# Kernel tuning notes

Measured on AMD Instinct MI355X. Metric: run time of the kernel, lower is better.

## Reference

```python
import jax, jax.numpy as jnp
import numpy as np

B, H, W, C = 64, 14, 14, 768

def setup_inputs() -> dict:
    key = jax.random.key(0)
    k = jax.random.split(key, 5)
    s = 0.02  # small init so tanh/sigmoid stay in active range
    return {
        "x": jax.random.normal(k[0], (B, H, W, C), dtype=jnp.float32),
        "Wx": jax.random.normal(k[1], (3 * C, C), dtype=jnp.float32) * s,
        "bx": jnp.zeros((3 * C,), dtype=jnp.float32),
        "Wh": jax.random.normal(k[2], (3 * C, C), dtype=jnp.float32) * s,
        "bh": jnp.zeros((3 * C,), dtype=jnp.float32),
        "Wp": jax.random.normal(k[3], (C, C), dtype=jnp.float32) * s,
    }

def reference(x, Wx, bx, Wh, bh, Wp):
    b, h_, w_, c = x.shape
    n = h_ * w_
    seq = x.reshape(b, n, c)
    # Input projections for all timesteps at once (no recurrent dependency).
    x_zrn = jnp.einsum('bnc,dc->bnd', seq, Wx) + bx  # [B, N, 3C]
    x_zrn_t = jnp.transpose(x_zrn, (1, 0, 2))        # [N, B, 3C] for scan

    def step(h, xz):
        h_zrn = h @ Wh.T + bh                         # [B, 3C]
        x_z, x_r, x_n = jnp.split(xz, 3, axis=-1)
        h_z, h_r, h_n = jnp.split(h_zrn, 3, axis=-1)
        z = jax.nn.sigmoid(x_z + h_z)
        r = jax.nn.sigmoid(x_r + h_r)
        ncand = jnp.tanh(x_n + r * h_n)
        h_new = (1.0 - z) * ncand + z * h
        return h_new, h_new

    h0 = jnp.zeros((b, c), dtype=x.dtype)
    _, hs = jax.lax.scan(step, h0, x_zrn_t)           # hs: [N, B, C]
    y = jnp.transpose(hs, (1, 0, 2))                  # [B, N, C]
    y = jnp.einsum('bnc,dc->bnd', y, Wp)              # proj (no bias)
    # proj_drop = 0.0 -> identity
    return y.reshape(b, h_, w_, c)
```

## Files before the change

kernel.cpp:

```cpp
#include <hip/hip_runtime.h>

typedef unsigned short u16;
typedef unsigned int   u32;
typedef unsigned long long u64;
typedef __attribute__((ext_vector_type(8))) short bf16x8;
typedef __attribute__((ext_vector_type(4))) float f32x4;

#define GK 768
#define NSTEP 196
#define HSTEP 49152
#define PWG 24
#define NGRP 8
#define NBLK 256
#define FLINE 32
#define FLAG0 64
#define MIR0 6656
#define GUARD (1 << 18)

__device__ __forceinline__ u16 f2bf(float f) {
    u32 u = __float_as_uint(f);
    u = (u + 0x7fffu + ((u >> 16) & 1u)) >> 16;
    return (u16)u;
}
__device__ __forceinline__ float bf2f(u16 h) { return __uint_as_float(((u32)h) << 16); }

__device__ __forceinline__ int agent_load(const int* p) {
    return __hip_atomic_load(p, __ATOMIC_RELAXED, __HIP_MEMORY_SCOPE_AGENT);
}
__device__ __forceinline__ void agent_store(int* p, int v) {
    __hip_atomic_store(p, v, __ATOMIC_RELAXED, __HIP_MEMORY_SCOPE_AGENT);
}
__device__ __forceinline__ int atomic_read_l2(int* p) {
    int v; int zero = 0;
    asm volatile("global_atomic_add %0, %1, %2, off sc0\n\t"
                 "s_waitcnt vmcnt(0)"
                 : "=&v"(v) : "v"(p), "v"(zero) : "memory");
    return v;
}

__global__ __launch_bounds__(256) void cvt_kernel(
    const float4* __restrict__ x, const float4* __restrict__ wx,
    const float4* __restrict__ wp,
    u32* __restrict__ xb, u32* __restrict__ wxb, u32* __restrict__ wpb,
    int* __restrict__ flags)
{
    const int N1 = 9633792 / 4, N2 = 1769472 / 4;
    int i = blockIdx.x * 256 + threadIdx.x;
    if (blockIdx.x < 32) flags[blockIdx.x * 256 + threadIdx.x] = 0;
    const float4* src; u32* dst; int off;
    if (i < N1)            { src = x;  dst = xb;  off = i; }
    else if (i < N1 + N2)  { src = wx; dst = wxb; off = i - N1; }
    else                   { src = wp; dst = wpb; off = i - N1 - N2; }
    float4 v = src[off];
    u32 lo = (u32)f2bf(v.x) | ((u32)f2bf(v.y) << 16);
    u32 hi = (u32)f2bf(v.z) | ((u32)f2bf(v.w) << 16);
    dst[(size_t)off * 2]     = lo;
    dst[(size_t)off * 2 + 1] = hi;
}

template<int MODE>
__global__ __launch_bounds__(256) void gemm_bt(
    const u16* __restrict__ A, const u16* __restrict__ B,
    const float* __restrict__ bias, void* __restrict__ outv)
{
    __shared__ u16 As[128 * 40];
    __shared__ u16 Bs[128 * 40];
    const int tid  = threadIdx.x;
    const int lane = tid & 63;
    const int wv   = tid >> 6;
    const int m0 = blockIdx.y * 128;
    const int n0 = blockIdx.x * 128;
    const int wm = (wv & 1) * 64;
    const int wn = (wv >> 1) * 64;

    f32x4 acc[4][4];
#pragma unroll
    for (int i = 0; i < 4; ++i)
#pragma unroll
        for (int j = 0; j < 4; ++j) acc[i][j] = (f32x4){0.f, 0.f, 0.f, 0.f};

    const int r0 = tid >> 2, q0 = tid & 3;
    const u16* gA0 = A + (size_t)(m0 + r0)      * GK + q0 * 8;
    const u16* gA1 = A + (size_t)(m0 + r0 + 64) * GK + q0 * 8;
    const u16* gB0 = B + (size_t)(n0 + r0)      * GK + q0 * 8;
    const u16* gB1 = B + (size_t)(n0 + r0 + 64) * GK + q0 * 8;
    u16* sA0 = As + r0 * 40 + q0 * 8;
    u16* sA1 = As + (r0 + 64) * 40 + q0 * 8;
    u16* sB0 = Bs + r0 * 40 + q0 * 8;
    u16* sB1 = Bs + (r0 + 64) * 40 + q0 * 8;

    const int fr = lane & 15, fq = lane >> 4;
    const u16* fA = As + (wm + fr) * 40 + fq * 8;
    const u16* fB = Bs + (wn + fr) * 40 + fq * 8;

    for (int kt = 0; kt < GK / 32; ++kt) {
        uint4 a0 = *(const uint4*)(gA0 + kt * 32);
        uint4 a1 = *(const uint4*)(gA1 + kt * 32);
        uint4 b0 = *(const uint4*)(gB0 + kt * 32);
        uint4 b1 = *(const uint4*)(gB1 + kt * 32);
        __syncthreads();
        *(uint4*)sA0 = a0; *(uint4*)sA1 = a1;
        *(uint4*)sB0 = b0; *(uint4*)sB1 = b1;
        __syncthreads();
        bf16x8 af[4], bfr[4];
#pragma unroll
        for (int mi = 0; mi < 4; ++mi) af[mi]  = *(const bf16x8*)(fA + mi * 16 * 40);
#pragma unroll
        for (int ni = 0; ni < 4; ++ni) bfr[ni] = *(const bf16x8*)(fB + ni * 16 * 40);
#pragma unroll
        for (int mi = 0; mi < 4; ++mi)
#pragma unroll
            for (int ni = 0; ni < 4; ++ni)
                acc[mi][ni] = __builtin_amdgcn_mfma_f32_16x16x32_bf16(
                    af[mi], bfr[ni], acc[mi][ni], 0, 0, 0);
    }

    if (MODE == 1) {
        u16* out = (u16*)outv;
#pragma unroll
        for (int mi = 0; mi < 4; ++mi) {
#pragma unroll
            for (int ni = 0; ni < 4; ++ni) {
                int col = n0 + wn + ni * 16 + fr;
                float bv = bias[col];
#pragma unroll
                for (int r = 0; r < 4; ++r) {
                    int m = m0 + wm + mi * 16 + fq * 4 + r;
                    int b = m / 196;
                    int nn = m - b * 196;
                    u16 hv = f2bf(acc[mi][ni][r] + bv);
                    int other = __shfl_xor((int)hv, 1, 64);
                    if (!(lane & 1)) {
                        u32 packed = (u32)hv | (((u32)(u16)other) << 16);
                        size_t eidx = ((size_t)nn * 64 + (size_t)b) * 2304 + (size_t)col;
                        *((u32*)out + (eidx >> 1)) = packed;
                    }
                }
            }
        }
    } else {
        float* out = (float*)outv;
#pragma unroll
        for (int mi = 0; mi < 4; ++mi) {
#pragma unroll
            for (int ni = 0; ni < 4; ++ni) {
                int col = n0 + wn + ni * 16 + fr;
#pragma unroll
                for (int r = 0; r < 4; ++r) {
                    int m = m0 + wm + mi * 16 + fq * 4 + r;
                    int b = m & 63;
                    int nn = m >> 6;
                    out[((size_t)b * 196 + nn) * 768 + col] = acc[mi][ni][r];
                }
            }
        }
    }
}

template<bool FAST>
__device__ void recur_core(
    int g, int s, int tid,
    const u16* __restrict__ xz, const float* __restrict__ Wh,
    const float* __restrict__ bh, u16* __restrict__ hsx, int* flags,
    float* hzs)
{
    const int lane = tid & 63;
    const int wv   = tid >> 6;
    const int kh   = wv & 1;
    const int np   = wv >> 1;
    const int fr   = lane & 15, fq = lane >> 4;
    const int c0   = s * 32;
    const int B0   = g * 8;

    bf16x8 bfrag[2][12];
#pragma unroll
    for (int j = 0; j < 2; ++j) {
        int row = np * 768 + c0 + j * 16 + fr;
        const float* wp = Wh + (size_t)row * 768 + kh * 384 + fq * 8;
#pragma unroll
        for (int kk = 0; kk < 12; ++kk) {
            float4 f0 = *(const float4*)(wp + kk * 32);
            float4 f1 = *(const float4*)(wp + kk * 32 + 4);
            bf16x8 b;
            b[0] = (short)f2bf(f0.x); b[1] = (short)f2bf(f0.y);
            b[2] = (short)f2bf(f0.z); b[3] = (short)f2bf(f0.w);
            b[4] = (short)f2bf(f1.x); b[5] = (short)f2bf(f1.y);
            b[6] = (short)f2bf(f1.z); b[7] = (short)f2bf(f1.w);
            bfrag[j][kk] = b;
        }
    }

    const int gb = tid >> 5, gi = tid & 31;
    const int gc = c0 + gi;
    float bh0 = 0.f, bh1 = 0.f, bh2 = 0.f, hold = 0.f;
    if (tid < 256) { bh0 = bh[gc]; bh1 = bh[768 + gc]; bh2 = bh[1536 + gc]; }

    const int pl = lane % PWG;
    int* const myflag = &flags[FLAG0 + (g * PWG + s)  * FLINE];
    int* const pollp  = &flags[FLAG0 + (g * PWG + pl) * FLINE];
    int* const mymir  = &flags[MIR0 + g * FLINE + s];
    const int* const pollm = &flags[MIR0 + g * FLINE + pl];

    float xgn0 = 0.f, xgn1 = 0.f, xgn2 = 0.f;
    if (tid < 256) {
        size_t xoff = (size_t)(B0 + gb) * 2304 + gc;
        xgn0 = bf2f(xz[xoff]);
        xgn1 = bf2f(xz[xoff + 768]);
        xgn2 = bf2f(xz[xoff + 1536]);
    }

    bool slow = !FAST;

    for (int n = 0; n < NSTEP; ++n) {
        const float xg0 = xgn0, xg1 = xgn1, xg2 = xgn2;

        f32x4 acc0 = (f32x4){0.f, 0.f, 0.f, 0.f};
        f32x4 acc1 = (f32x4){0.f, 0.f, 0.f, 0.f};

        if (n > 0) {
            if (tid >= 320) {
                bool done = false;
                if (FAST && !slow) {
                    int tries = 0;
                    for (;;) {
                        int v = atomic_read_l2(pollp);
                        if (__all(v >= n)) { done = true; break; }
                        if (++tries > 4096) { slow = true; break; }
                        __builtin_amdgcn_s_sleep(1);
                    }
                }
                if (!done) {
                    int guard = 0;
                    for (;;) {
                        int v = agent_load(pollm);
                        if (__all(v >= n)) break;
                        if (++guard > GUARD) break;
                        __builtin_amdgcn_s_sleep(1);
                    }
                }
            }
            __syncthreads();

            const u16* ap = hsx + (size_t)(n - 1) * HSTEP
                                + (size_t)(B0 + fr) * 768 + kh * 384 + fq * 8;
            const bool arow = fr < 8;
#pragma unroll
            for (int kk = 0; kk < 12; ++kk) {
                bf16x8 a = arow ? *(const bf16x8*)(ap + kk * 32)
                                : (bf16x8){0, 0, 0, 0, 0, 0, 0, 0};
                acc0 = __builtin_amdgcn_mfma_f32_16x16x32_bf16(a, bfrag[0][kk], acc0, 0, 0, 0);
                acc1 = __builtin_amdgcn_mfma_f32_16x16x32_bf16(a, bfrag[1][kk], acc1, 0, 0, 0);
            }
        }

#pragma unroll
        for (int r = 0; r < 4; ++r) {
            int b = fq * 4 + r;
            if (b < 8) {
                hzs[(kh * 8 + b) * 96 + np * 32 + fr]      = acc0[r];
                hzs[(kh * 8 + b) * 96 + np * 32 + 16 + fr] = acc1[r];
            }
        }
        __syncthreads();

        if (tid < 256) {
            float h0 = hzs[gb * 96 + gi]      + hzs[(8 + gb) * 96 + gi]      + bh0;
            float h1 = hzs[gb * 96 + 32 + gi] + hzs[(8 + gb) * 96 + 32 + gi] + bh1;
            float h2 = hzs[gb * 96 + 64 + gi] + hzs[(8 + gb) * 96 + 64 + gi] + bh2;
            float z   = 1.f / (1.f + __expf(-(xg0 + h0)));
            float rr2 = 1.f / (1.f + __expf(-(xg1 + h1)));
            float pre = xg2 + rr2 * h2;
            float e2  = __expf(-2.f * pre);
            float nc  = (1.f - e2) / (1.f + e2);
            float hnew = (1.f - z) * nc + z * hold;
            hold = hnew;

            u16 hv = f2bf(hnew);
            u32 other = ((u32)__shfl_xor((int)hv, 1, 64)) & 0xffffu;
            u32 v01 = (u32)hv | (other << 16);
            u32 v23 = (u32)__shfl_xor((int)v01, 2, 64);
            if ((tid & 3) == 0) {
                u64 q = (u64)v01 | ((u64)v23 << 32);
                size_t ofs = (size_t)n * HSTEP + (size_t)(B0 + gb) * 768 + gc;
                u64* p = (u64*)(hsx + ofs);
                *p = q;
                __hip_atomic_store(p, q, __ATOMIC_RELAXED,
                                   __HIP_MEMORY_SCOPE_AGENT);
            }
        }
        asm volatile("s_waitcnt vmcnt(0)" ::: "memory");
        __syncthreads();
        if (tid == 0)       *myflag = n + 1;
        else if (tid == 64) agent_store(mymir, n + 1);

        if (tid < 256) {
            int np1 = (n + 1 < NSTEP) ? n + 1 : NSTEP - 1;
            size_t xoff = ((size_t)np1 * 64 + (B0 + gb)) * 2304 + gc;
            xgn0 = bf2f(xz[xoff]);
            xgn1 = bf2f(xz[xoff + 768]);
            xgn2 = bf2f(xz[xoff + 1536]);
        }
    }
}

__global__ __launch_bounds__(384) void recur4_kernel(
    const u16* __restrict__ xz, const float* __restrict__ Wh,
    const float* __restrict__ bh, u16* __restrict__ hsx, int* flags)
{
    __shared__ float hzs[2 * 8 * 96];
    __shared__ int sh_mode, sh_g, sh_s;
    const int tid = threadIdx.x;

    __builtin_amdgcn_fence(__ATOMIC_ACQUIRE, "agent");

    if (tid == 0) {
        u32 xcc = 0;
        asm volatile("s_getreg_b32 %0, hwreg(HW_REG_XCC_ID)" : "=s"(xcc));
        const int my_xcd = (int)(xcc & 7u);
        const int slot = __hip_atomic_fetch_add(&flags[my_xcd], 1, __ATOMIC_ACQ_REL,
                                                __HIP_MEMORY_SCOPE_AGENT);
        __hip_atomic_fetch_add(&flags[15], 1, __ATOMIC_ACQ_REL,
                               __HIP_MEMORY_SCOPE_AGENT);
        int guard = 0;
        while (__hip_atomic_load(&flags[15], __ATOMIC_ACQUIRE,
                                 __HIP_MEMORY_SCOPE_AGENT) < NBLK) {
            if (++guard > GUARD) break;
            __builtin_amdgcn_s_sleep(1);
        }
        int G = 0, pre = 0, myg = 0;
        for (int x = 0; x < 8; ++x) {
            int c  = agent_load(&flags[x]);
            int gx = c / PWG;
            if (x < my_xcd) pre += gx;
            if (x == my_xcd) myg = gx;
            G += gx;
        }
        const int grp = pre + slot / PWG;
        const bool act = (slot < myg * PWG) && (grp < NGRP);
        sh_mode = (G >= NGRP) ? (act ? 1 : 2) : 0;
        sh_g = grp;
        sh_s = slot % PWG;
    }
    __syncthreads();
    const int mode = sh_mode;

    if (mode == 1) {
        recur_core<true>(sh_g, sh_s, tid, xz, Wh, bh, hsx, flags, hzs);
    } else if (mode == 0) {
        const int bid = blockIdx.x;
        if (bid < NGRP * PWG)
            recur_core<false>(bid / PWG, bid % PWG, tid, xz, Wh, bh, hsx,
                              flags, hzs);
    }
}

extern "C" void kernel_launch(void* const* d_in, const int* in_sizes, int n_in,
                              void* d_out, int out_size, void* d_ws, size_t ws_size,
                              hipStream_t stream)
{
    const float* x  = (const float*)d_in[0];
    const float* Wx = (const float*)d_in[1];
    const float* bx = (const float*)d_in[2];
    const float* Wh = (const float*)d_in[3];
    const float* bh = (const float*)d_in[4];
    const float* Wp = (const float*)d_in[5];
    float* out = (float*)d_out;

    char* ws = (char*)d_ws;
    size_t off = 0;
    auto wsalloc = [&](size_t bytes) -> void* {
        void* p = ws + off;
        off += (bytes + 255) & ~(size_t)255;
        return p;
    };
    u16* xb   = (u16*)wsalloc(9633792ull * 2);
    u16* wxb  = (u16*)wsalloc(1769472ull * 2);
    u16* wpb  = (u16*)wsalloc(589824ull * 2);
    u16* xzrn = (u16*)wsalloc(196ull * 64 * 2304 * 2);
    u16* hsx  = (u16*)wsalloc(196ull * 64 * 768 * 2);
    int* flags = (int*)wsalloc(32768);

    cvt_kernel<<<11712, 256, 0, stream>>>(
        (const float4*)x, (const float4*)Wx, (const float4*)Wp,
        (u32*)xb, (u32*)wxb, (u32*)wpb, flags);

    gemm_bt<1><<<dim3(18, 98), 256, 0, stream>>>(xb, wxb, bx, (void*)xzrn);

    {
        const u16* a0 = xzrn; const float* a1 = Wh; const float* a2 = bh;
        u16* a3 = hsx; int* a4 = flags;
        void* args[5] = { &a0, &a1, &a2, &a3, &a4 };
        hipLaunchCooperativeKernel((void*)recur4_kernel, dim3(NBLK), dim3(384),
                                   args, 0, stream);
    }

    gemm_bt<0><<<dim3(6, 98), 256, 0, stream>>>(hsx, wpb, nullptr, (void*)out);
}
```

Before: 1.174 ms.

## Replace per-block step flags with per-group atomic counter barrier

Each of the 24 blocks in a group used to publish its step number to its own flag line, and 64 lanes polled all 24 flags. Now each block atomically increments one shared counter per group, and a single thread polls it until it reaches n*PWG, with a longer sleep and more tries. The fast path also drops the duplicate atomic store of hidden-state data and keeps only the plain store. The aim is less polling traffic and fewer stores per step. In exchange, all 24 blocks now contend on one counter line, and correctness relies on the plain store plus the wait still making data visible across XCDs.

Result: no change. 1.177 ms (+0.3%).

```diff
diff --git a/kernel.cpp b/kernel.cpp
--- a/kernel.cpp
+++ b/kernel.cpp
@@ -24,18 +24,17 @@
 }
 __device__ __forceinline__ float bf2f(u16 h) { return __uint_as_float(((u32)h) << 16); }
 
-__device__ __forceinline__ int agent_load(const int* p) {
-    return __hip_atomic_load(p, __ATOMIC_RELAXED, __HIP_MEMORY_SCOPE_AGENT);
-}
-__device__ __forceinline__ void agent_store(int* p, int v) {
-    __hip_atomic_store(p, v, __ATOMIC_RELAXED, __HIP_MEMORY_SCOPE_AGENT);
-}
 __device__ __forceinline__ int atomic_read_l2(int* p) {
     int v; int zero = 0;
     asm volatile("global_atomic_add %0, %1, %2, off sc0\n\t"
                  "s_waitcnt vmcnt(0)"
                  : "=&v"(v) : "v"(p), "v"(zero) : "memory");
     return v;
+}
+__device__ __forceinline__ void atomic_inc_l2(int* p) {
+    int one = 1;
+    asm volatile("global_atomic_add %0, %1, off"
+                 :: "v"(p), "v"(one) : "memory");
 }
 
 __global__ __launch_bounds__(256) void cvt_kernel(
@@ -195,11 +194,8 @@
     float bh0 = 0.f, bh1 = 0.f, bh2 = 0.f, hold = 0.f;
     if (tid < 256) { bh0 = bh[gc]; bh1 = bh[768 + gc]; bh2 = bh[1536 + gc]; }
 
-    const int pl = lane % PWG;
-    int* const myflag = &flags[FLAG0 + (g * PWG + s)  * FLINE];
-    int* const pollp  = &flags[FLAG0 + (g * PWG + pl) * FLINE];
-    int* const mymir  = &flags[MIR0 + g * FLINE + s];
-    const int* const pollm = &flags[MIR0 + g * FLINE + pl];
+    int* const mycnt = &flags[FLAG0 + g * FLINE];
+    int* const mymir = &flags[MIR0 + g * FLINE];
 
     float xgn0 = 0.f, xgn1 = 0.f, xgn2 = 0.f;
     if (tid < 256) {
@@ -218,24 +214,23 @@
         f32x4 acc1 = (f32x4){0.f, 0.f, 0.f, 0.f};
 
         if (n > 0) {
-            if (tid >= 320) {
-                bool done = false;
-                if (FAST && !slow) {
+            if (tid == 320) {
+                const int need = n * PWG;
+                if (!slow) {
                     int tries = 0;
                     for (;;) {
-                        int v = atomic_read_l2(pollp);
-                        if (__all(v >= n)) { done = true; break; }
-                        if (++tries > 4096) { slow = true; break; }
-                        __builtin_amdgcn_s_sleep(1);
+                        int v = atomic_read_l2(mycnt);
+                        if (v >= need) break;
+                        if (++tries > 8192) { slow = true; break; }
+                        __builtin_amdgcn_s_sleep(2);
                     }
                 }
-                if (!done) {
+                if (slow) {
                     int guard = 0;
-                    for (;;) {
-                        int v = agent_load(pollm);
-                        if (__all(v >= n)) break;
+                    while (__hip_atomic_load(mymir, __ATOMIC_RELAXED,
+                                             __HIP_MEMORY_SCOPE_AGENT) < need) {
                         if (++guard > GUARD) break;
-                        __builtin_amdgcn_s_sleep(1);
+                        __builtin_amdgcn_s_sleep(2);
                     }
                 }
             }
@@ -283,15 +278,25 @@
                 u64 q = (u64)v01 | ((u64)v23 << 32);
                 size_t ofs = (size_t)n * HSTEP + (size_t)(B0 + gb) * 768 + gc;
                 u64* p = (u64*)(hsx + ofs);
-                *p = q;
-                __hip_atomic_store(p, q, __ATOMIC_RELAXED,
-                                   __HIP_MEMORY_SCOPE_AGENT);
+                if (FAST) {
+                    *p = q;
+                } else {
+                    __hip_atomic_store(p, q, __ATOMIC_RELAXED,
+                                       __HIP_MEMORY_SCOPE_AGENT);
+                }
             }
         }
         asm volatile("s_waitcnt vmcnt(0)" ::: "memory");
         __syncthreads();
-        if (tid == 0)       *myflag = n + 1;
-        else if (tid == 64) agent_store(mymir, n + 1);
+        if (FAST) {
+            if (tid == 0)       atomic_inc_l2(mycnt);
+            else if (tid == 64) __hip_atomic_fetch_add(mymir, 1,
+                                    __ATOMIC_RELAXED,
+                                    __HIP_MEMORY_SCOPE_AGENT);
+        } else {
+            if (tid == 0) __hip_atomic_fetch_add(mymir, 1,
+                              __ATOMIC_RELAXED, __HIP_MEMORY_SCOPE_AGENT);
+        }
 
         if (tid < 256) {
             int np1 = (n + 1 < NSTEP) ? n + 1 : NSTEP - 1;
@@ -303,7 +308,7 @@
     }
 }
 
-__global__ __launch_bounds__(384) void recur4_kernel(
+__global__ __launch_bounds__(384) void recur5_kernel(
     const u16* __restrict__ xz, const float* __restrict__ Wh,
     const float* __restrict__ bh, u16* __restrict__ hsx, int* flags)
 {
@@ -329,7 +334,8 @@
         }
         int G = 0, pre = 0, myg = 0;
         for (int x = 0; x < 8; ++x) {
-            int c  = agent_load(&flags[x]);
+            int c  = __hip_atomic_load(&flags[x], __ATOMIC_RELAXED,
+                                       __HIP_MEMORY_SCOPE_AGENT);
             int gx = c / PWG;
             if (x < my_xcd) pre += gx;
             if (x == my_xcd) myg = gx;
@@ -390,7 +396,7 @@
         const u16* a0 = xzrn; const float* a1 = Wh; const float* a2 = bh;
         u16* a3 = hsx; int* a4 = flags;
         void* args[5] = { &a0, &a1, &a2, &a3, &a4 };
-        hipLaunchCooperativeKernel((void*)recur4_kernel, dim3(NBLK), dim3(384),
+        hipLaunchCooperativeKernel((void*)recur5_kernel, dim3(NBLK), dim3(384),
                                    args, 0, stream);
     }
 
```
